# Kernel tuning notes

Measured on AMD Instinct MI355X. Metric: run time of the kernel, lower is better.

## Reference

```python
import jax, jax.numpy as jnp
import numpy as np
from jax.scipy.special import logsumexp

B, T, D = 256, 2048, 64


def setup_inputs() -> dict:
    key = jax.random.key(0)
    k1, k2, k3, k4 = jax.random.split(key, 4)
    p = jax.random.normal(k1, (B, T, D), dtype=jnp.float32)
    labels = jax.random.randint(k2, (B, T), 0, D)
    y = jax.nn.one_hot(labels, D, dtype=jnp.int32)  # [B,T,D] one-hot labels
    # valid lengths in [T//2, T]; mask == 1 marks padding positions
    lengths = jax.random.randint(k3, (B,), T // 2, T + 1)
    mask = (jnp.arange(T)[None, :] >= lengths[:, None]).astype(jnp.int32)
    transition = 0.1 * jax.random.normal(k4, (D, D), dtype=jnp.float32)
    return {"p": p, "y": y, "mask": mask, "transition": transition}


def reference(p, y, mask, transition):
    # CRF negative log-likelihood per example: logZ - emission_score - transition_score
    Bb = p.shape[0]
    valid = (1 - mask).astype(jnp.float32)            # [B,T], 1 = valid token
    y1 = y.astype(jnp.float32) * valid[:, :, None]    # masked one-hot labels
    s1 = jnp.sum(y1 * p, axis=(1, 2))                 # emission score
    pair = jnp.einsum('btd,bte->bde', y1[:, :-1], y1[:, 1:])  # label bigram counts
    s2 = jnp.sum(pair * transition, axis=(1, 2))      # transition score

    # forward algorithm: alpha_t = p_t + logsumexp(alpha_{t-1}[:, :, None] + T)
    def step(state, inp):
        new = inp + logsumexp(state[:, :, None] + transition[None, :, :], axis=1)
        return new, new

    xs = jnp.moveaxis(p[:, 1:, :], 1, 0)              # [T-1, B, D]
    _, a1 = jax.lax.scan(step, p[:, 0, :], xs)        # a1: [T-1, B, D]

    # index of alpha at the last valid timestep (length L -> a1 index L-2)
    m1 = jnp.argmin(
        jnp.concatenate([valid.astype(jnp.int32), jnp.zeros((Bb, 1), jnp.int32)], axis=1),
        axis=1) - 2                                   # [B]
    last = a1[m1, jnp.arange(Bb)]                     # [B, D]
    logZ = logsumexp(last, axis=-1)
    return logZ - s1 - s2
```

## Files before the change

kernel.cpp:

```cpp
#include <hip/hip_runtime.h>
#include <stdint.h>
#include <string.h>

#define BB 256
#define TT 2048
#define DD 64
#define C_L2E 1.44269504f
#define C_LN2 0.69314718f
#define C_BIAS 0.0028174f

typedef short sh8  __attribute__((ext_vector_type(8)));
typedef float f32x4 __attribute__((ext_vector_type(4)));

union BU { sh8 v8; unsigned int u[4]; unsigned short s[8]; };

__device__ __forceinline__ float expf_fast(float x) { return __builtin_amdgcn_exp2f(x * C_L2E); }
__device__ __forceinline__ unsigned short bf16rne(float x) {
    unsigned int u = __float_as_uint(x);
    u += 0x7FFF + ((u >> 16) & 1u);
    return (unsigned short)(u >> 16);
}
__device__ __forceinline__ unsigned int pkbf(float hi, float lo) {
    return __builtin_amdgcn_perm(__float_as_uint(hi), __float_as_uint(lo), 0x07060302u);
}

#define DPPMAX(x, ctrl, rm, bm) { int _xi = __float_as_int(x);                              \
    int _yi = __builtin_amdgcn_update_dpp(_xi, _xi, ctrl, rm, bm, false);                   \
    x = fmaxf(x, __int_as_float(_yi)); }

__global__ __launch_bounds__(256) void crf_score(
    const float* __restrict__ p, const int* __restrict__ y,
    const int* __restrict__ mask, const float* __restrict__ tr,
    float* __restrict__ wsS, int* __restrict__ wsL)
{
    __shared__ unsigned char labs[257];
    __shared__ float redf[4];
    __shared__ int redi[4];
    const int c = blockIdx.y, t0 = blockIdx.x * 256;
    const int tid = threadIdx.x;
    const int t = t0 + tid;

    const int mv = mask[(size_t)c * TT + t];
    float s1 = 0.f, s2 = 0.f;
    int vc = (mv == 0) ? 1 : 0;
    if (mv == 0) {
        const int4* yt = (const int4*)y + ((size_t)c * TT + t) * 16;
        int lab = 0;
#pragma unroll
        for (int g = 0; g < 16; ++g) {
            int4 v = yt[g];
            if (v.x) lab = 4 * g;     if (v.y) lab = 4 * g + 1;
            if (v.z) lab = 4 * g + 2; if (v.w) lab = 4 * g + 3;
        }
        labs[tid] = (unsigned char)lab;
        s1 = p[((size_t)c * TT + t) * DD + lab];
    }
    if (tid == 0) {
        int tb = t0 + 256;
        if (tb < TT && mask[(size_t)c * TT + tb] == 0) {
            const int4* yt = (const int4*)y + ((size_t)c * TT + tb) * 16;
            int lab = 0;
#pragma unroll
            for (int g = 0; g < 16; ++g) {
                int4 v = yt[g];
                if (v.x) lab = 4 * g;     if (v.y) lab = 4 * g + 1;
                if (v.z) lab = 4 * g + 2; if (v.w) lab = 4 * g + 3;
            }
            labs[256] = (unsigned char)lab;
        }
    }
    __syncthreads();
    if (t + 1 < TT && mask[(size_t)c * TT + t + 1] == 0)
        s2 = tr[(int)labs[tid] * DD + (int)labs[tid + 1]];

    float acc = s1 + s2;
#pragma unroll
    for (int xm = 32; xm >= 1; xm >>= 1) { acc += __shfl_xor(acc, xm, 64); vc += __shfl_xor(vc, xm, 64); }
    if ((tid & 63) == 0) { redf[tid >> 6] = acc; redi[tid >> 6] = vc; }
    __syncthreads();
    if (tid == 0) {
        atomicAdd(&wsS[c], redf[0] + redf[1] + redf[2] + redf[3]);
        atomicAdd(&wsL[c], redi[0] + redi[1] + redi[2] + redi[3]);
    }
}

__global__ __launch_bounds__(256) void crf_probe(
    const float* __restrict__ p, const float* __restrict__ tr,
    const int* __restrict__ wsL,
    float* __restrict__ wsA, float* __restrict__ wsB, int* __restrict__ wsSig)
{
    const int tid = threadIdx.x, w = tid >> 6, lane = tid & 63;
    const int q = lane >> 4, ml = lane & 15;
    const int cg = blockIdx.x;
    const int ic = blockIdx.y * 4 + w;
    const int bwd = blockIdx.z;
    const int c = cg * 16 + ml;
    const int Lml = wsL[c];
    const int t0 = ic * 128, t1 = t0 + 128;
    const int ts = (ic == 0) ? 1 : t0;
    const float* prow = p + (size_t)c * TT * DD;

    BU A[4][2];
#pragma unroll
    for (int mt = 0; mt < 4; ++mt)
#pragma unroll
        for (int kt2 = 0; kt2 < 2; ++kt2)
#pragma unroll
            for (int j = 0; j < 8; ++j) {
                int lam = 32 * kt2 + 16 * (j >> 2) + 4 * q + (j & 3);
                float tv = bwd ? tr[(16 * mt + ml) * DD + lam] : tr[lam * DD + 16 * mt + ml];
                A[mt][kt2].s[j] = (short)bf16rne(expf_fast(tv));
            }

    float xs[16];
    if (!bwd && ic == 0) {
#pragma unroll
        for (int k = 0; k < 4; ++k) {
            f32x4 v = *(const f32x4*)(prow + 16 * k + 4 * q);
#pragma unroll
            for (int r = 0; r < 4; ++r)
                xs[(k >> 1) * 8 + (k & 1) * 4 + r] = __builtin_amdgcn_exp2f(fmaf(v[r], C_L2E, C_BIAS));
        }
    } else {
#pragma unroll
        for (int i = 0; i < 16; ++i) xs[i] = 1.0f;
    }

    int mL = Lml;
#pragma unroll
    for (int xm = 32; xm >= 1; xm >>= 1) { int o = __shfl_xor(mL, xm, 64); mL = o > mL ? o : mL; }
    int ibeg = 0, iend = 128;
    if (!bwd) { int ir = mL - t0; if (ir < 0) ir = 0; iend = (ir + 3) & ~3; if (iend > 128) iend = 128; }
    else      { int ir = t1 - mL; if (ir < 0) ir = 0; ibeg = ir & ~3; if (ibeg > 128) ibeg = 128; }

    int sig = 0;
    const f32x4 z4 = {0.f, 0.f, 0.f, 0.f};

    if (ibeg < iend) {
        f32x4 er[4][4];
#pragma unroll
        for (int s = 0; s < 4; ++s) {
            int i = ibeg + s;
            int t = bwd ? (t1 - 1 - i) : (t0 + i);
#pragma unroll
            for (int k = 0; k < 4; ++k)
                er[s][k] = *(const f32x4*)(prow + (size_t)t * DD + 16 * k + 4 * q);
        }
        for (int ib = ibeg; ib < iend; ib += 4) {
#pragma unroll
            for (int s = 0; s < 4; ++s) {
                const int i = ib + s;
                const int t = bwd ? (t1 - 1 - i) : (t0 + i);
                const bool act = (t >= ts) && (t < Lml);
                float ee[4][4];
#pragma unroll
                for (int k = 0; k < 4; ++k)
#pragma unroll
                    for (int r = 0; r < 4; ++r)
                        ee[k][r] = __builtin_amdgcn_exp2f(fmaf(er[s][k][r], C_L2E, C_BIAS));
                {
                    int ipf = i + 4;
                    int tpf = bwd ? (t1 - 1 - ipf) : (t0 + ipf);
                    if (tpf < t0) tpf = t0;
                    if (tpf > t1 - 1) tpf = t1 - 1;
#pragma unroll
                    for (int k = 0; k < 4; ++k)
                        er[s][k] = *(const f32x4*)(prow + (size_t)tpf * DD + 16 * k + 4 * q);
                }
                float cand[16];
                BU Bf[2];
                f32x4 acc[4];
                if (!bwd) {
#pragma unroll
                    for (int kt2 = 0; kt2 < 2; ++kt2)
#pragma unroll
                        for (int jj = 0; jj < 4; ++jj)
                            Bf[kt2].u[jj] = pkbf(xs[kt2 * 8 + 2 * jj + 1], xs[kt2 * 8 + 2 * jj]);
#pragma unroll
                    for (int mt = 0; mt < 4; ++mt) {
                        acc[mt] = __builtin_amdgcn_mfma_f32_16x16x32_bf16(A[mt][0].v8, Bf[0].v8, z4, 0, 0, 0);
                        acc[mt] = __builtin_amdgcn_mfma_f32_16x16x32_bf16(A[mt][1].v8, Bf[1].v8, acc[mt], 0, 0, 0);
                    }
#pragma unroll
                    for (int mt = 0; mt < 4; ++mt)
#pragma unroll
                        for (int r = 0; r < 4; ++r)
                            cand[(mt >> 1) * 8 + (mt & 1) * 4 + r] = acc[mt][r] * ee[mt][r];
                } else {
                    float xsc[16];
#pragma unroll
                    for (int kt2 = 0; kt2 < 2; ++kt2)
#pragma unroll
                        for (int h = 0; h < 2; ++h)
#pragma unroll
                            for (int r = 0; r < 4; ++r)
                                xsc[kt2 * 8 + h * 4 + r] = xs[kt2 * 8 + h * 4 + r] * ee[2 * kt2 + h][r];
#pragma unroll
                    for (int kt2 = 0; kt2 < 2; ++kt2)
#pragma unroll
                        for (int jj = 0; jj < 4; ++jj)
                            Bf[kt2].u[jj] = pkbf(xsc[kt2 * 8 + 2 * jj + 1], xsc[kt2 * 8 + 2 * jj]);
#pragma unroll
                    for (int mt = 0; mt < 4; ++mt) {
                        acc[mt] = __builtin_amdgcn_mfma_f32_16x16x32_bf16(A[mt][0].v8, Bf[0].v8, z4, 0, 0, 0);
                        acc[mt] = __builtin_amdgcn_mfma_f32_16x16x32_bf16(A[mt][1].v8, Bf[1].v8, acc[mt], 0, 0, 0);
                    }
#pragma unroll
                    for (int mt = 0; mt < 4; ++mt)
#pragma unroll
                        for (int r = 0; r < 4; ++r)
                            cand[(mt >> 1) * 8 + (mt & 1) * 4 + r] = acc[mt][r];
                }
                if (s == 3) {
                    float mx = fabsf(cand[0]);
#pragma unroll
                    for (int i2 = 1; i2 < 16; ++i2) mx = fmaxf(mx, fabsf(cand[i2]));
                    DPPMAX(mx, 0x111, 0xF, 0xF); DPPMAX(mx, 0x112, 0xF, 0xF);
                    DPPMAX(mx, 0x114, 0xF, 0xF); DPPMAX(mx, 0x118, 0xF, 0xF);
                    DPPMAX(mx, 0x142, 0xA, 0xF); DPPMAX(mx, 0x143, 0xC, 0xF);
                    int smx = __builtin_amdgcn_readlane(__float_as_int(mx), 63);
                    int kk = ((smx >> 23) & 255) - 127;
                    kk = kk < -124 ? -124 : (kk > 124 ? 124 : kk);
                    float sc = __int_as_float((unsigned)(127 - kk) << 23);
#pragma unroll
                    for (int i2 = 0; i2 < 16; ++i2) cand[i2] *= sc;
                    if (act) sig += kk;
                }
#pragma unroll
                for (int i2 = 0; i2 < 16; ++i2) xs[i2] = act ? cand[i2] : xs[i2];
            }
        }
    }

    float* dst = (bwd ? wsB : wsA) + ((size_t)c * 16 + ic) * 64;
#pragma unroll
    for (int kt2 = 0; kt2 < 2; ++kt2)
#pragma unroll
        for (int h = 0; h < 2; ++h)
#pragma unroll
            for (int r = 0; r < 4; ++r)
                dst[32 * kt2 + 16 * h + 4 * q + r] = xs[kt2 * 8 + h * 4 + r];
    if (!bwd && q == 0) wsSig[c * 16 + ic] = sig;
}

__global__ __launch_bounds__(256) void crf_combine(
    const float* __restrict__ wsA, const float* __restrict__ wsB,
    const int* __restrict__ wsSig, const float* __restrict__ wsS,
    float* __restrict__ out)
{
    const int tid = threadIdx.x, w = tid >> 6, lane = tid & 63;
    const int c = blockIdx.x * 4 + w;
    float a[16], b[16];
#pragma unroll
    for (int i = 0; i < 16; ++i) {
        a[i] = wsA[((size_t)c * 16 + i) * 64 + lane];
        b[i] = wsB[((size_t)c * 16 + i) * 64 + lane];
    }
    float E = (float)wsSig[c * 16];
    float curl = a[0];
#pragma unroll
    for (int i = 1; i < 16; ++i) {
        float d1 = b[i] * curl;
        float d0 = b[i];
#pragma unroll
        for (int xm = 32; xm >= 1; xm >>= 1) { d1 += __shfl_xor(d1, xm, 64); d0 += __shfl_xor(d0, xm, 64); }
        E += (float)wsSig[c * 16 + i] + __builtin_amdgcn_logf(d1) - __builtin_amdgcn_logf(d0);
        curl = a[i];
    }
    float sum = curl;
#pragma unroll
    for (int xm = 32; xm >= 1; xm >>= 1) sum += __shfl_xor(sum, xm, 64);
    float logZ = C_LN2 * (__builtin_amdgcn_logf(sum) + E);
    if (lane == 0) out[c] = logZ - wsS[c];
}

extern "C" void kernel_launch(void* const* d_in, const int* in_sizes, int n_in,
                              void* d_out, int out_size, void* d_ws, size_t ws_size,
                              hipStream_t stream) {
    const float* p  = (const float*)d_in[0];
    const int*   y  = (const int*)d_in[1];
    const int*   mk = (const int*)d_in[2];
    const float* tr = (const float*)d_in[3];
    float* out = (float*)d_out;

    float* wsS  = (float*)d_ws;
    int*   wsL  = (int*)((char*)d_ws + 1024);
    int*   wsSg = (int*)((char*)d_ws + 2048);
    float* wsA  = (float*)((char*)d_ws + 32768);
    float* wsB  = (float*)((char*)d_ws + 32768 + (1u << 20));

    hipMemsetAsync(d_ws, 0, 2048, stream);
    crf_score<<<dim3(8, BB), dim3(256), 0, stream>>>(p, y, mk, tr, wsS, wsL);
    crf_probe<<<dim3(16, 4, 2), dim3(256), 0, stream>>>(p, tr, wsL, wsA, wsB, wsSg);
    crf_combine<<<dim3(BB / 4), dim3(256), 0, stream>>>(wsA, wsB, wsSg, wsS, out);
}
```

Measured before the change: 336.8 us.

## Split CRF forward scan into more chunks with bf16 workspace and parallel combine

After: 317.5 us. -5.7%, faster.

```diff
diff --git a/kernel.cpp b/kernel.cpp
--- a/kernel.cpp
+++ b/kernel.cpp
@@ -5,6 +5,8 @@
 #define BB 256
 #define TT 2048
 #define DD 64
+#define CC 64
+#define SS 32
 #define C_L2E 1.44269504f
 #define C_LN2 0.69314718f
 #define C_BIAS 0.0028174f
@@ -33,44 +35,53 @@
     const int* __restrict__ mask, const float* __restrict__ tr,
     float* __restrict__ wsS, int* __restrict__ wsL)
 {
+    __shared__ int mk[257];
     __shared__ unsigned char labs[257];
     __shared__ float redf[4];
     __shared__ int redi[4];
     const int c = blockIdx.y, t0 = blockIdx.x * 256;
     const int tid = threadIdx.x;
-    const int t = t0 + tid;
-
-    const int mv = mask[(size_t)c * TT + t];
-    float s1 = 0.f, s2 = 0.f;
-    int vc = (mv == 0) ? 1 : 0;
-    if (mv == 0) {
-        const int4* yt = (const int4*)y + ((size_t)c * TT + t) * 16;
-        int lab = 0;
-#pragma unroll
-        for (int g = 0; g < 16; ++g) {
-            int4 v = yt[g];
-            if (v.x) lab = 4 * g;     if (v.y) lab = 4 * g + 1;
-            if (v.z) lab = 4 * g + 2; if (v.w) lab = 4 * g + 3;
-        }
-        labs[tid] = (unsigned char)lab;
-        s1 = p[((size_t)c * TT + t) * DD + lab];
-    }
-    if (tid == 0) {
-        int tb = t0 + 256;
-        if (tb < TT && mask[(size_t)c * TT + tb] == 0) {
-            const int4* yt = (const int4*)y + ((size_t)c * TT + tb) * 16;
-            int lab = 0;
-#pragma unroll
-            for (int g = 0; g < 16; ++g) {
-                int4 v = yt[g];
-                if (v.x) lab = 4 * g;     if (v.y) lab = 4 * g + 1;
-                if (v.z) lab = 4 * g + 2; if (v.w) lab = 4 * g + 3;
+    const int g = tid & 15, sub = tid >> 4;
+    const size_t cb = (size_t)c * TT;
+
+    mk[tid] = mask[cb + t0 + tid];
+    if (tid == 0) mk[256] = (t0 + 256 < TT) ? mask[cb + t0 + 256] : 1;
+    __syncthreads();
+
+    float s1 = 0.f;
+    int vc = 0;
+#pragma unroll
+    for (int k = 0; k < 16; ++k) {
+        const int ti = k * 16 + sub;
+        if (mk[ti] == 0) {
+            int4 v = ((const int4*)y)[(cb + t0 + ti) * 16 + g];
+            int cand = v.w ? 4 * g + 3 : v.z ? 4 * g + 2 : v.y ? 4 * g + 1 : v.x ? 4 * g : -1;
+#pragma unroll
+            for (int xm = 1; xm <= 8; xm <<= 1) {
+                int o = __shfl_xor(cand, xm, 16);
+                cand = o > cand ? o : cand;
             }
-            labs[256] = (unsigned char)lab;
-        }
+            if (g == 0) {
+                labs[ti] = (unsigned char)cand;
+                s1 += p[(cb + t0 + ti) * DD + cand];
+                vc += 1;
+            }
+        }
+    }
+    if (tid < 16 && mk[256] == 0) {
+        int4 v = ((const int4*)y)[(cb + t0 + 256) * 16 + tid];
+        int cand = v.w ? 4 * tid + 3 : v.z ? 4 * tid + 2 : v.y ? 4 * tid + 1 : v.x ? 4 * tid : -1;
+#pragma unroll
+        for (int xm = 1; xm <= 8; xm <<= 1) {
+            int o = __shfl_xor(cand, xm, 16);
+            cand = o > cand ? o : cand;
+        }
+        if (tid == 0) labs[256] = (unsigned char)cand;
     }
     __syncthreads();
-    if (t + 1 < TT && mask[(size_t)c * TT + t + 1] == 0)
+
+    float s2 = 0.f;
+    if (mk[tid + 1] == 0)
         s2 = tr[(int)labs[tid] * DD + (int)labs[tid + 1]];
 
     float acc = s1 + s2;
@@ -87,16 +98,16 @@
 __global__ __launch_bounds__(256) void crf_probe(
     const float* __restrict__ p, const float* __restrict__ tr,
     const int* __restrict__ wsL,
-    float* __restrict__ wsA, float* __restrict__ wsB, int* __restrict__ wsSig)
+    unsigned short* __restrict__ wsA, unsigned short* __restrict__ wsB, int* __restrict__ wsSig)
 {
     const int tid = threadIdx.x, w = tid >> 6, lane = tid & 63;
     const int q = lane >> 4, ml = lane & 15;
     const int cg = blockIdx.x;
-    const int ic = blockIdx.y * 4 + w;
-    const int bwd = blockIdx.z;
+    const int ic = blockIdx.y * 2 + (w >> 1);
+    const int bwd = w & 1;
     const int c = cg * 16 + ml;
     const int Lml = wsL[c];
-    const int t0 = ic * 128, t1 = t0 + 128;
+    const int t0 = ic * SS, t1 = t0 + SS;
     const int ts = (ic == 0) ? 1 : t0;
     const float* prow = p + (size_t)c * TT * DD;
 
@@ -129,9 +140,9 @@
     int mL = Lml;
 #pragma unroll
     for (int xm = 32; xm >= 1; xm >>= 1) { int o = __shfl_xor(mL, xm, 64); mL = o > mL ? o : mL; }
-    int ibeg = 0, iend = 128;
-    if (!bwd) { int ir = mL - t0; if (ir < 0) ir = 0; iend = (ir + 3) & ~3; if (iend > 128) iend = 128; }
-    else      { int ir = t1 - mL; if (ir < 0) ir = 0; ibeg = ir & ~3; if (ibeg > 128) ibeg = 128; }
+    int ibeg = 0, iend = SS;
+    if (!bwd) { int ir = mL - t0; if (ir < 0) ir = 0; iend = (ir + 3) & ~3; if (iend > SS) iend = SS; }
+    else      { int ir = t1 - mL; if (ir < 0) ir = 0; ibeg = ir & ~3; if (ibeg > SS) ibeg = SS; }
 
     int sig = 0;
     const f32x4 z4 = {0.f, 0.f, 0.f, 0.f};
@@ -232,46 +243,51 @@
         }
     }
 
-    float* dst = (bwd ? wsB : wsA) + ((size_t)c * 16 + ic) * 64;
+    unsigned short* dst = (bwd ? wsB : wsA) + ((size_t)c * CC + ic) * 64;
 #pragma unroll
     for (int kt2 = 0; kt2 < 2; ++kt2)
 #pragma unroll
         for (int h = 0; h < 2; ++h)
 #pragma unroll
             for (int r = 0; r < 4; ++r)
-                dst[32 * kt2 + 16 * h + 4 * q + r] = xs[kt2 * 8 + h * 4 + r];
-    if (!bwd && q == 0) wsSig[c * 16 + ic] = sig;
+                dst[32 * kt2 + 16 * h + 4 * q + r] = bf16rne(xs[kt2 * 8 + h * 4 + r]);
+    if (!bwd && q == 0) wsSig[c * CC + ic] = sig;
 }
 
 __global__ __launch_bounds__(256) void crf_combine(
-    const float* __restrict__ wsA, const float* __restrict__ wsB,
+    const unsigned short* __restrict__ wsA, const unsigned short* __restrict__ wsB,
     const int* __restrict__ wsSig, const float* __restrict__ wsS,
     float* __restrict__ out)
 {
+    __shared__ float eParts[4];
     const int tid = threadIdx.x, w = tid >> 6, lane = tid & 63;
-    const int c = blockIdx.x * 4 + w;
-    float a[16], b[16];
-#pragma unroll
-    for (int i = 0; i < 16; ++i) {
-        a[i] = wsA[((size_t)c * 16 + i) * 64 + lane];
-        b[i] = wsB[((size_t)c * 16 + i) * 64 + lane];
-    }
-    float E = (float)wsSig[c * 16];
-    float curl = a[0];
-#pragma unroll
-    for (int i = 1; i < 16; ++i) {
-        float d1 = b[i] * curl;
-        float d0 = b[i];
+    const int c = blockIdx.x;
+
+    float Ep = 0.f;
+#pragma unroll
+    for (int k = 0; k < 16; ++k) {
+        const int i = w * 16 + k;
+        if (i == 0) continue;
+        float b  = __uint_as_float((unsigned)wsB[((size_t)c * CC + i) * 64 + lane] << 16);
+        float ap = __uint_as_float((unsigned)wsA[((size_t)c * CC + i - 1) * 64 + lane] << 16);
+        float d1 = b * ap, d0 = b;
 #pragma unroll
         for (int xm = 32; xm >= 1; xm >>= 1) { d1 += __shfl_xor(d1, xm, 64); d0 += __shfl_xor(d0, xm, 64); }
-        E += (float)wsSig[c * 16 + i] + __builtin_amdgcn_logf(d1) - __builtin_amdgcn_logf(d0);
-        curl = a[i];
-    }
-    float sum = curl;
-#pragma unroll
-    for (int xm = 32; xm >= 1; xm >>= 1) sum += __shfl_xor(sum, xm, 64);
-    float logZ = C_LN2 * (__builtin_amdgcn_logf(sum) + E);
-    if (lane == 0) out[c] = logZ - wsS[c];
+        Ep += (float)wsSig[c * CC + i] + __builtin_amdgcn_logf(d1) - __builtin_amdgcn_logf(d0);
+    }
+    if (w == 0) Ep += (float)wsSig[c * CC];
+    if (w == 3) {
+        float al = __uint_as_float((unsigned)wsA[((size_t)c * CC + CC - 1) * 64 + lane] << 16);
+#pragma unroll
+        for (int xm = 32; xm >= 1; xm >>= 1) al += __shfl_xor(al, xm, 64);
+        Ep += __builtin_amdgcn_logf(al);
+    }
+    if (lane == 0) eParts[w] = Ep;
+    __syncthreads();
+    if (tid == 0) {
+        float E = eParts[0] + eParts[1] + eParts[2] + eParts[3];
+        out[c] = C_LN2 * E - wsS[c];
+    }
 }
 
 extern "C" void kernel_launch(void* const* d_in, const int* in_sizes, int n_in,
@@ -286,11 +302,11 @@
     float* wsS  = (float*)d_ws;
     int*   wsL  = (int*)((char*)d_ws + 1024);
     int*   wsSg = (int*)((char*)d_ws + 2048);
-    float* wsA  = (float*)((char*)d_ws + 32768);
-    float* wsB  = (float*)((char*)d_ws + 32768 + (1u << 20));
+    unsigned short* wsA = (unsigned short*)((char*)d_ws + 131072);
+    unsigned short* wsB = (unsigned short*)((char*)d_ws + 131072 + (2u << 20));
 
     hipMemsetAsync(d_ws, 0, 2048, stream);
     crf_score<<<dim3(8, BB), dim3(256), 0, stream>>>(p, y, mk, tr, wsS, wsL);
-    crf_probe<<<dim3(16, 4, 2), dim3(256), 0, stream>>>(p, tr, wsL, wsA, wsB, wsSg);
-    crf_combine<<<dim3(BB / 4), dim3(256), 0, stream>>>(wsA, wsB, wsSg, wsS, out);
-}
+    crf_probe<<<dim3(16, CC / 2), dim3(256), 0, stream>>>(p, tr, wsL, wsA, wsB, wsSg);
+    crf_combine<<<dim3(BB), dim3(256), 0, stream>>>(wsA, wsB, wsSg, wsS, out);
+}
```
